# Kernel optimization log

Measured on AMD Instinct MI355X. Metric: run time of the kernel, lower is better.

The kernel has to match this reference:

```python
import jax, jax.numpy as jnp
import numpy as np

NUM_UNITS = 64
IN_FEATURES = 256
OUT_FEATURES = 256


def _uw(x, w):
    # per-unit linear: x [B,U,I], w [U,I,O] -> [B,U,O]
    return jnp.einsum('bui,uio->buo', x, w)


def setup_inputs() -> dict:
    key = jax.random.key(0)
    ks = jax.random.split(key, 8)
    bound = float(np.sqrt(1.0 / OUT_FEATURES))
    U, I, O = NUM_UNITS, IN_FEATURES, OUT_FEATURES
    B = 256
    uni = lambda k, s: jax.random.uniform(k, s, jnp.float32, -bound, bound)
    return {
        'x': jax.random.normal(ks[0], (B, U, I), jnp.float32),
        'w_ir': uni(ks[1], (U, I, O)),
        'w_iz': uni(ks[2], (U, I, O)),
        'w_in': uni(ks[3], (U, I, O)),
        'w_hr': uni(ks[4], (U, O, O)),
        'w_hz': uni(ks[5], (U, O, O)),
        'w_hn': uni(ks[6], (U, O, O)),
        'hidden_init': uni(ks[7], (1, U, O)),
    }


def reference(x, w_ir, w_iz, w_in, w_hr, w_hz, w_hn, hidden_init):
    # hidden initialized by broadcasting hidden_init over batch (first call)
    h = jnp.broadcast_to(hidden_init, (x.shape[0],) + hidden_init.shape[1:])
    r = jax.nn.sigmoid(_uw(x, w_ir) + _uw(h, w_hr))
    z = jax.nn.sigmoid(_uw(x, w_iz) + _uw(h, w_hz))
    n = jnp.tanh(_uw(x, w_in) + r * _uw(h, w_hn))
    return (1.0 - z) * n + z * h
```

## Files before the change

kernel.cpp:

```cpp
#include <hip/hip_runtime.h>
#include <hip/hip_bf16.h>

#define UNITS 64
#define IFEAT 256
#define OFEAT 256

typedef __attribute__((ext_vector_type(8))) short v8s;
typedef __attribute__((ext_vector_type(4))) float v4f;

static __device__ __forceinline__ unsigned int pk2(float a, float b) {
    union { __hip_bfloat162 h; unsigned int u; } c;
    c.h = __float22bfloat162_rn(float2{a, b});
    return c.u;
}

static __device__ __forceinline__ float sigmoid_f(float x) {
    return 1.0f / (1.0f + __expf(-x));
}
static __device__ __forceinline__ float tanh_f(float x) {
    float ax = fabsf(x);
    float e = __expf(-2.0f * ax);
    float t = (1.0f - e) / (1.0f + e);
    return copysignf(t, x);
}

__global__ __launch_bounds__(512, 8) void gru_hvec(
        const float* __restrict__ whr,
        const float* __restrict__ whz,
        const float* __restrict__ whn,
        const float* __restrict__ hinit,
        float* __restrict__ hv) {
    __shared__ float red[512];
    const int bid  = blockIdx.x;
    const int half = bid & 1;
    const int u    = (bid >> 1) & 63;
    const int w    = bid >> 7;
    const float* wh = (w == 0) ? whr : (w == 1) ? whz : whn;

    const int t = threadIdx.x;
    const int o = half * 128 + (t & 127);
    const int c = t >> 7;
    const float* hp = hinit + u * IFEAT;
    const float* wp = wh + (size_t)u * IFEAT * OFEAT + o;

    float acc = 0.0f;
    const int i0 = c * 64;
#pragma unroll 8
    for (int i = 0; i < 64; ++i) {
        acc += hp[i0 + i] * wp[(size_t)(i0 + i) * OFEAT];
    }
    red[t] = acc;
    __syncthreads();
    if (c == 0)
        hv[((size_t)w * UNITS + u) * OFEAT + o] =
            red[t] + red[t + 128] + red[t + 256] + red[t + 384];
}

__global__ __launch_bounds__(1024, 4) void gru_gemm(
    const float* __restrict__ x,
    const float* __restrict__ wir,
    const float* __restrict__ wiz,
    const float* __restrict__ win,
    const float* __restrict__ hinit,
    const float* __restrict__ hv,
    float* __restrict__ out) {
    __shared__ unsigned short As[32][128][8];
    __shared__ unsigned short Bs[2][3][4][128][8];

    const int bid = blockIdx.x;
    const int idx = bid >> 3;
    const int u   = (bid & 7) * 8 + (idx >> 2);
    const int rem = idx & 3;
    const int b0  = (rem >> 1) * 128;
    const int o0  = (rem & 1) * 128;

    const int t    = threadIdx.x;
    const int lane = t & 63;
    const int wv   = t >> 6;
    const int wm   = wv >> 2;
    const int wn   = wv & 3;
    const int lg   = lane >> 4;
    const int lr   = lane & 15;

    const int bcol = t & 127;
    const int bkq  = (t >> 7) & 3;
    const int gA   = t >> 9;
    const bool hasB = (wv < 8);
    const float* wpA = (gA == 0) ? wir : wiz;
    const size_t bgbase = (size_t)u * (IFEAT * OFEAT) + (bkq * 8) * OFEAT + o0 + bcol;

    float rbA[8], rbB[8];

    auto bload = [&](int kk) {
        const size_t off = bgbase + (size_t)kk * 32 * OFEAT;
#pragma unroll
        for (int j = 0; j < 8; ++j) rbA[j] = wpA[off + j * OFEAT];
        if (hasB) {
#pragma unroll
            for (int j = 0; j < 8; ++j) rbB[j] = win[off + j * OFEAT];
        }
    };
    auto bwrite = [&](int bb) {
        uint4 v;
        v.x = pk2(rbA[0], rbA[1]);
        v.y = pk2(rbA[2], rbA[3]);
        v.z = pk2(rbA[4], rbA[5]);
        v.w = pk2(rbA[6], rbA[7]);
        *(uint4*)&Bs[bb][gA][bkq][bcol][0] = v;
        if (hasB) {
            uint4 w;
            w.x = pk2(rbB[0], rbB[1]);
            w.y = pk2(rbB[2], rbB[3]);
            w.z = pk2(rbB[4], rbB[5]);
            w.w = pk2(rbB[6], rbB[7]);
            *(uint4*)&Bs[bb][2][bkq][bcol][0] = w;
        }
    };

    v4f acc[3][2][2];
#pragma unroll
    for (int g = 0; g < 3; ++g)
#pragma unroll
        for (int mi = 0; mi < 2; ++mi)
#pragma unroll
            for (int ni = 0; ni < 2; ++ni)
                acc[g][mi][ni] = (v4f){0.f, 0.f, 0.f, 0.f};

    bload(0);
    {
        const int kqA = lane >> 1;
        const int j0  = (lane & 1) * 4;
#pragma unroll
        for (int i = 0; i < 8; ++i) {
            const int row = wv * 8 + i;
            v4f q = *(const v4f*)(x + (size_t)(b0 + row) * (UNITS * IFEAT)
                                    + u * IFEAT + lane * 4);
            uint2 w;
            w.x = pk2(q[0], q[1]);
            w.y = pk2(q[2], q[3]);
            *(uint2*)&As[kqA][(row + kqA) & 127][j0] = w;
        }
    }
    bwrite(0);
    bload(1);
    __syncthreads();

#pragma unroll
    for (int kk = 0; kk < 8; ++kk) {
        const int bb = kk & 1;
        if (kk < 7) bwrite(bb ^ 1);
        if (kk < 6) bload(kk + 2);

        const int kq0 = kk * 4 + lg;
        v8s a0 = *(const v8s*)&As[kq0][((wm * 32 + lr) + kq0) & 127][0];
        v8s a1 = *(const v8s*)&As[kq0][((wm * 32 + 16 + lr) + kq0) & 127][0];
#pragma unroll
        for (int g = 0; g < 3; ++g) {
#pragma unroll
            for (int ni = 0; ni < 2; ++ni) {
                v8s b = *(const v8s*)&Bs[bb][g][lg][wn * 32 + ni * 16 + lr][0];
                acc[g][0][ni] = __builtin_amdgcn_mfma_f32_16x16x32_bf16(a0, b, acc[g][0][ni], 0, 0, 0);
                acc[g][1][ni] = __builtin_amdgcn_mfma_f32_16x16x32_bf16(a1, b, acc[g][1][ni], 0, 0, 0);
            }
        }
        if (kk < 7) __syncthreads();
    }

    const int obase = o0 + wn * 32 + lr;
    float hrv[2], hzv[2], hnv[2], h0v[2];
#pragma unroll
    for (int ni = 0; ni < 2; ++ni) {
        const int o = obase + ni * 16;
        hrv[ni] = hv[(0 * UNITS + u) * OFEAT + o];
        hzv[ni] = hv[(1 * UNITS + u) * OFEAT + o];
        hnv[ni] = hv[(2 * UNITS + u) * OFEAT + o];
        h0v[ni] = hinit[u * OFEAT + o];
    }
    const int rbase = b0 + wm * 32 + lg * 4;
#pragma unroll
    for (int mi = 0; mi < 2; ++mi) {
#pragma unroll
        for (int ni = 0; ni < 2; ++ni) {
            const int o = obase + ni * 16;
#pragma unroll
            for (int jj = 0; jj < 4; ++jj) {
                const int row = rbase + mi * 16 + jj;
                const float r = sigmoid_f(acc[0][mi][ni][jj] + hrv[ni]);
                const float z = sigmoid_f(acc[1][mi][ni][jj] + hzv[ni]);
                const float n = tanh_f(acc[2][mi][ni][jj] + r * hnv[ni]);
                out[((size_t)row * UNITS + u) * OFEAT + o] = (1.0f - z) * n + z * h0v[ni];
            }
        }
    }
}

extern "C" void kernel_launch(void* const* d_in, const int* in_sizes, int n_in,
                              void* d_out, int out_size, void* d_ws, size_t ws_size,
                              hipStream_t stream) {
    const float* x     = (const float*)d_in[0];
    const float* w_ir  = (const float*)d_in[1];
    const float* w_iz  = (const float*)d_in[2];
    const float* w_in  = (const float*)d_in[3];
    const float* w_hr  = (const float*)d_in[4];
    const float* w_hz  = (const float*)d_in[5];
    const float* w_hn  = (const float*)d_in[6];
    const float* hinit = (const float*)d_in[7];
    float* out = (float*)d_out;
    float* hv  = (float*)d_ws;

    gru_hvec<<<dim3(384), dim3(512), 0, stream>>>(w_hr, w_hz, w_hn, hinit, hv);
    gru_gemm<<<dim3(256), dim3(1024), 0, stream>>>(x, w_ir, w_iz, w_in, hinit, hv, out);
}
```

Measured before the change: 34.67 us.

## Fuse hidden-state matvec into the GEMM kernel and drop the separate launch

Removes the standalone gru_hvec kernel and has each GEMM block compute its own h·W_h slice for the gates. The partial sums go into shared memory and are reduced during the second K iteration, overlapping the GEMM pipeline. This saves a kernel launch and the global round trip through the workspace. In exchange, blocks that share a unit read the same hidden weights twice, and the prologue gets longer before the MFMA loop starts.

Result: slower. 45.15 us (+30.2%).

```diff
diff --git a/kernel.cpp b/kernel.cpp
--- a/kernel.cpp
+++ b/kernel.cpp
@@ -24,48 +24,20 @@
     return copysignf(t, x);
 }
 
-__global__ __launch_bounds__(512, 8) void gru_hvec(
-        const float* __restrict__ whr,
-        const float* __restrict__ whz,
-        const float* __restrict__ whn,
-        const float* __restrict__ hinit,
-        float* __restrict__ hv) {
-    __shared__ float red[512];
-    const int bid  = blockIdx.x;
-    const int half = bid & 1;
-    const int u    = (bid >> 1) & 63;
-    const int w    = bid >> 7;
-    const float* wh = (w == 0) ? whr : (w == 1) ? whz : whn;
-
-    const int t = threadIdx.x;
-    const int o = half * 128 + (t & 127);
-    const int c = t >> 7;
-    const float* hp = hinit + u * IFEAT;
-    const float* wp = wh + (size_t)u * IFEAT * OFEAT + o;
-
-    float acc = 0.0f;
-    const int i0 = c * 64;
-#pragma unroll 8
-    for (int i = 0; i < 64; ++i) {
-        acc += hp[i0 + i] * wp[(size_t)(i0 + i) * OFEAT];
-    }
-    red[t] = acc;
-    __syncthreads();
-    if (c == 0)
-        hv[((size_t)w * UNITS + u) * OFEAT + o] =
-            red[t] + red[t + 128] + red[t + 256] + red[t + 384];
-}
-
-__global__ __launch_bounds__(1024, 4) void gru_gemm(
+__global__ __launch_bounds__(1024, 4) void gru_fused(
     const float* __restrict__ x,
     const float* __restrict__ wir,
     const float* __restrict__ wiz,
     const float* __restrict__ win,
+    const float* __restrict__ whr,
+    const float* __restrict__ whz,
+    const float* __restrict__ whn,
     const float* __restrict__ hinit,
-    const float* __restrict__ hv,
     float* __restrict__ out) {
     __shared__ unsigned short As[32][128][8];
     __shared__ unsigned short Bs[2][3][4][128][8];
+    __shared__ float Ph[8][3][128];
+    __shared__ float Hf[3][128];
 
     const int bid = blockIdx.x;
     const int idx = bid >> 3;
@@ -143,11 +115,39 @@
     }
     bwrite(0);
     bload(1);
+
+    {
+        const int ho = t & 127;
+        const int hq = t >> 7;
+        const float* hp = hinit + u * IFEAT + hq * 32;
+        const size_t whbase = (size_t)u * (IFEAT * OFEAT)
+                            + (size_t)(hq * 32) * OFEAT + o0 + ho;
+        float p0 = 0.f, p1 = 0.f, p2 = 0.f;
+#pragma unroll
+        for (int i = 0; i < 32; ++i) {
+            const float hi = hp[i];
+            const size_t off = whbase + (size_t)i * OFEAT;
+            p0 += hi * whr[off];
+            p1 += hi * whz[off];
+            p2 += hi * whn[off];
+        }
+        Ph[hq][0][ho] = p0;
+        Ph[hq][1][ho] = p1;
+        Ph[hq][2][ho] = p2;
+    }
+
     __syncthreads();
 
 #pragma unroll
     for (int kk = 0; kk < 8; ++kk) {
         const int bb = kk & 1;
+        if (kk == 1 && t < 384) {
+            const int g = t >> 7, o = t & 127;
+            float s = 0.f;
+#pragma unroll
+            for (int q = 0; q < 8; ++q) s += Ph[q][g][o];
+            Hf[g][o] = s;
+        }
         if (kk < 7) bwrite(bb ^ 1);
         if (kk < 6) bload(kk + 2);
 
@@ -166,16 +166,16 @@
         if (kk < 7) __syncthreads();
     }
 
+    float hrv[2], hzv[2], hnv[2], h0v[2];
+#pragma unroll
+    for (int ni = 0; ni < 2; ++ni) {
+        const int ol = wn * 32 + ni * 16 + lr;
+        hrv[ni] = Hf[0][ol];
+        hzv[ni] = Hf[1][ol];
+        hnv[ni] = Hf[2][ol];
+        h0v[ni] = hinit[u * OFEAT + o0 + ol];
+    }
     const int obase = o0 + wn * 32 + lr;
-    float hrv[2], hzv[2], hnv[2], h0v[2];
-#pragma unroll
-    for (int ni = 0; ni < 2; ++ni) {
-        const int o = obase + ni * 16;
-        hrv[ni] = hv[(0 * UNITS + u) * OFEAT + o];
-        hzv[ni] = hv[(1 * UNITS + u) * OFEAT + o];
-        hnv[ni] = hv[(2 * UNITS + u) * OFEAT + o];
-        h0v[ni] = hinit[u * OFEAT + o];
-    }
     const int rbase = b0 + wm * 32 + lg * 4;
 #pragma unroll
     for (int mi = 0; mi < 2; ++mi) {
@@ -206,8 +206,7 @@
     const float* w_hn  = (const float*)d_in[6];
     const float* hinit = (const float*)d_in[7];
     float* out = (float*)d_out;
-    float* hv  = (float*)d_ws;
-
-    gru_hvec<<<dim3(384), dim3(512), 0, stream>>>(w_hr, w_hz, w_hn, hinit, hv);
-    gru_gemm<<<dim3(256), dim3(1024), 0, stream>>>(x, w_ir, w_iz, w_in, hinit, hv, out);
-}
+
+    gru_fused<<<dim3(256), dim3(1024), 0, stream>>>(
+        x, w_ir, w_iz, w_in, w_hr, w_hz, w_hn, hinit, out);
+}
```
